# Performance work log

Measured on AMD Instinct MI355X. Metric: run time of the kernel, lower is better.

Reference implementation:

```python
import jax, jax.numpy as jnp
import numpy as np

NE = 64        # num experts
H = 1024       # hidden_size
F = 2048       # ffn_hidden_size per expert
T = 16384      # total tokens


def setup_inputs() -> dict:
    key = jax.random.key(0)
    k1, k2, k3 = jax.random.split(key, 3)
    x = jax.random.normal(k1, (T, H), jnp.float32)
    w1 = jax.random.normal(k2, (NE, F, H), jnp.float32) * 0.02
    w2 = jax.random.normal(k3, (NE, F, H), jnp.float32) * 0.02
    # ragged token counts per expert, summing exactly to T
    rng = np.random.default_rng(0)
    sizes = rng.multinomial(T, np.ones(NE) / NE)
    tokens_per_expert = jnp.asarray(sizes, jnp.int32)
    return {"x": x, "w1": w1, "w2": w2, "tokens_per_expert": tokens_per_expert}


def _grouped_gmm(x, w, sizes, trans_b=False):
    # grouped GEMM: per-expert segment of x multiplied by that expert's weight.
    # sizes are concrete host ints (group boundaries are static), so we emit
    # one GEMM per expert with static slices, matching gg.ops.gmm semantics.
    offs = np.concatenate([[0], np.cumsum(sizes)]).astype(np.int64)
    outs = []
    for e in range(len(sizes)):
        xe = x[int(offs[e]):int(offs[e + 1])]          # [n_e, k]
        we = w[e].T if trans_b else w[e]               # [k, n]
        outs.append(xe @ we)
    return jnp.concatenate(outs, axis=0)


def reference(x, w1, w2, tokens_per_expert):
    sizes = np.asarray(tokens_per_expert)
    h = _grouped_gmm(x, w1, sizes, trans_b=True)       # [T, F]
    h = jax.nn.gelu(h, approximate=False)              # torch F.gelu (exact erf)
    return _grouped_gmm(h, w2, sizes, trans_b=False)   # [T, H]
```

## Files before the change

### kernel.cpp

```cpp
#include <hip/hip_runtime.h>
#include <hip/hip_bf16.h>

#define NE 64
#define HDIM 1024
#define FDIM 2048
#define TDIM 16384

typedef __attribute__((ext_vector_type(8))) short short8;
typedef __attribute__((ext_vector_type(4))) float f32x4;
typedef unsigned short u16;
typedef unsigned int u32;

struct IC0 { static constexpr int v = 0; };
struct IC1 { static constexpr int v = 1; };

__device__ __forceinline__ u16 f2bf(float f) {
  return __bfloat16_as_ushort(__float2bfloat16(f));
}
__device__ __forceinline__ u32 pk2(float a, float b) {
  return (u32)f2bf(a) | ((u32)f2bf(b) << 16);
}
template<int N> __device__ __forceinline__ void waitv() {
  if constexpr (N == 2)       asm volatile("s_waitcnt vmcnt(2)" ::: "memory");
  else if constexpr (N == 4)  asm volatile("s_waitcnt vmcnt(4)" ::: "memory");
  else if constexpr (N == 8)  asm volatile("s_waitcnt vmcnt(8)" ::: "memory");
  else if constexpr (N == 10) asm volatile("s_waitcnt vmcnt(10)" ::: "memory");
}
__device__ __forceinline__ void waitl() {
  asm volatile("s_waitcnt lgkmcnt(0)" ::: "memory");
}

__global__ void k_prep(const int* __restrict__ tpe, int4* __restrict__ map,
                       int* __restrict__ nblocks) {
  if (threadIdx.x != 0 || blockIdx.x != 0) return;
  int off = 0, nb = 0;
  for (int e = 0; e < NE; ++e) {
    int n = tpe[e];
    for (int r = 0; r < n; r += 256) {
      int re = (r + 256 < n) ? (r + 256) : n;
      map[nb++] = make_int4(e, off + r, off + re, 0);
    }
    off += n;
  }
  *nblocks = nb;
}

__global__ void k_conv(const float4* __restrict__ in, uint2* __restrict__ out, int n4) {
  int stride = gridDim.x * blockDim.x;
  for (int i = blockIdx.x * blockDim.x + threadIdx.x; i < n4; i += stride) {
    float4 v = in[i];
    uint2 o;
    o.x = pk2(v.x, v.y);
    o.y = pk2(v.z, v.w);
    out[i] = o;
  }
}

template<int K, int N, bool GELU, int BMODE, int NY>
__global__ __launch_bounds__(512) void k_gemm(
    const u16* __restrict__ A, const float* __restrict__ Bf, void* __restrict__ C,
    const int4* __restrict__ map, const int* __restrict__ nblocks)
{
  const int mblk = (int)blockIdx.x / NY;
  const int nblk = (int)blockIdx.x % NY;
  if (mblk >= *nblocks) return;
  const int4 mi = map[mblk];
  const int e = mi.x, row0 = mi.y, rowend = mi.z;
  const int n0 = nblk << 7;
  const int NT = K / 32;
  constexpr int LB = (BMODE == 1) ? 2 : 8;

  __shared__ __align__(16) u16 sa[2][8192];
  __shared__ __align__(16) u16 sb[128 * 40];

  const int tid = threadIdx.x;
  const int wid = tid >> 6, lane = tid & 63;
  const int wr = wid >> 1, wc = wid & 1;
  const int fr = lane & 15, fq = lane >> 4;

  f32x4 acc[4][4];
#pragma unroll
  for (int m = 0; m < 4; ++m)
#pragma unroll
    for (int n = 0; n < 4; ++n) acc[m][n] = (f32x4)0.f;

  const float* B = Bf + (size_t)e * ((size_t)N * K);

  float4 rb1[2][2];
  float  rb2[2][8];
  const int bn  = tid & 127;
  const int oct = tid >> 7;

  auto issueA = [&](int t) {
    const int buf = t & 1;
#pragma unroll
    for (int i = 0; i < 2; ++i) {
      int slot = i * 512 + tid;
      int row = row0 + (slot >> 2);
      row = row < TDIM ? row : TDIM - 1;
      const u16* g = A + (size_t)row * K + t * 32 + (slot & 3) * 8;
      __builtin_amdgcn_global_load_lds(
          (const __attribute__((address_space(1))) u32*)g,
          (__attribute__((address_space(3))) u32*)(&sa[buf][i * 4096 + wid * 512]),
          16, 0, 0);
    }
  };
  auto loadB = [&](int t, auto ic) {
    constexpr int S = decltype(ic)::v;
    if constexpr (BMODE == 1) {
#pragma unroll
      for (int i = 0; i < 2; ++i) {
        int slot = i * 512 + tid;
        rb1[S][i] = *(const float4*)(B + (size_t)(n0 + (slot >> 3)) * K + t * 32 + (slot & 7) * 4);
      }
    } else {
      const float* src = B + (size_t)(t * 32 + oct * 8) * N + n0 + bn;
#pragma unroll
      for (int i = 0; i < 8; ++i) rb2[S][i] = src[(size_t)i * N];
    }
  };
  auto writeB = [&](auto ic) {
    constexpr int S = decltype(ic)::v;
    if constexpr (BMODE == 1) {
#pragma unroll
      for (int i = 0; i < 2; ++i) {
        int slot = i * 512 + tid;
        uint2 o;
        o.x = pk2(rb1[S][i].x, rb1[S][i].y);
        o.y = pk2(rb1[S][i].z, rb1[S][i].w);
        *(uint2*)(&sb[(slot >> 3) * 40 + (slot & 7) * 4]) = o;
      }
    } else {
      uint4 c;
      c.x = pk2(rb2[S][0], rb2[S][1]); c.y = pk2(rb2[S][2], rb2[S][3]);
      c.z = pk2(rb2[S][4], rb2[S][5]); c.w = pk2(rb2[S][6], rb2[S][7]);
      *(uint4*)(&sb[bn * 40 + oct * 8]) = c;
    }
  };

  auto body = [&](int t, auto icCur) {
    waitv<2 + LB>();
    waitl();
    __builtin_amdgcn_s_barrier();
    const int cur = t & 1;
    short8 av[4], bv[4];
#pragma unroll
    for (int m = 0; m < 4; ++m)
      av[m] = *(const short8*)(&sa[cur][(wr * 64 + m * 16 + fr) * 32 + fq * 8]);
#pragma unroll
    for (int n = 0; n < 4; ++n)
      bv[n] = *(const short8*)(&sb[(wc * 64 + n * 16 + fr) * 40 + fq * 8]);
    waitl();
    __builtin_amdgcn_sched_barrier(0);
    __builtin_amdgcn_s_barrier();
    if (t + 2 < NT) issueA(t + 2);
    if (t + 1 < NT) writeB(icCur);
    if (t + 3 < NT) loadB(t + 3, icCur);
    __builtin_amdgcn_sched_barrier(0);
#pragma unroll
    for (int m = 0; m < 4; ++m)
#pragma unroll
      for (int n = 0; n < 4; ++n)
        acc[m][n] = __builtin_amdgcn_mfma_f32_16x16x32_bf16(av[m], bv[n], acc[m][n], 0, 0, 0);
  };

  issueA(0);
  loadB(0, IC0{});
  loadB(1, IC1{});
  waitv<LB>();
  writeB(IC0{});
  issueA(1);
  loadB(2, IC0{});
  for (int t = 0; t < NT; t += 2) {
    body(t, IC1{});
    body(t + 1, IC0{});
  }

#pragma unroll
  for (int m = 0; m < 4; ++m) {
    const int rb = row0 + wr * 64 + m * 16 + fq * 4;
#pragma unroll
    for (int n = 0; n < 4; ++n) {
      const int col = n0 + wc * 64 + n * 16 + fr;
#pragma unroll
      for (int j = 0; j < 4; ++j) {
        int r = rb + j;
        if (r < rowend) {
          float vv = acc[m][n][j];
          if constexpr (GELU) {
            vv = 0.5f * vv * (1.f + erff(vv * 0.70710678118654752f));
            ((u16*)C)[(size_t)r * N + col] = f2bf(vv);
          } else {
            ((float*)C)[(size_t)r * N + col] = vv;
          }
        }
      }
    }
  }
}

extern "C" void kernel_launch(void* const* d_in, const int* in_sizes, int n_in,
                              void* d_out, int out_size, void* d_ws, size_t ws_size,
                              hipStream_t stream) {
  const float* x  = (const float*)d_in[0];
  const float* w1 = (const float*)d_in[1];
  const float* w2 = (const float*)d_in[2];
  const int*  tpe = (const int*)d_in[3];

  char* ws = (char*)d_ws;
  int4* map     = (int4*)ws;
  int*  nblocks = (int*)(ws + 4096);
  u16*  xb      = (u16*)(ws + 8192);
  u16*  hb      = xb + (size_t)TDIM * HDIM;

  k_prep<<<1, 64, 0, stream>>>(tpe, map, nblocks);
  k_conv<<<2048, 256, 0, stream>>>((const float4*)x, (uint2*)xb, (TDIM * HDIM) / 4);
  k_gemm<HDIM, FDIM, true,  1, 16><<<128 * 16, 512, 0, stream>>>(
      xb, w1, (void*)hb, map, nblocks);
  k_gemm<FDIM, HDIM, false, 2, 8><<<128 * 8, 512, 0, stream>>>(
      hb, w2, d_out, map, nblocks);
}
```

Measured before the change: 540.5 us.

## Double-buffer B tile, swizzle A LDS layout, drop mid-iteration barrier

Makes the B shared-memory tile double-buffered so the next B tile can be written while the current one is read. This removes the second barrier and lgkm wait inside each K iteration. The A tile now gets a prefetch distance of one instead of two, and its LDS layout is XOR-swizzled on both the global_load_lds writes and the fragment reads to reduce bank conflicts. Out-of-range prefetches are clamped to the last tile instead of skipped. This trades extra LDS use and redundant tail loads for fewer synchronization points. The reduced A lookahead and removed barrier raise the risk of read/write races on the shared buffers.

Measured after the change: 517.5 us. 4.3% less time.

```diff
diff --git a/kernel.cpp b/kernel.cpp
--- a/kernel.cpp
+++ b/kernel.cpp
@@ -22,9 +22,7 @@
 }
 template<int N> __device__ __forceinline__ void waitv() {
   if constexpr (N == 2)       asm volatile("s_waitcnt vmcnt(2)" ::: "memory");
-  else if constexpr (N == 4)  asm volatile("s_waitcnt vmcnt(4)" ::: "memory");
   else if constexpr (N == 8)  asm volatile("s_waitcnt vmcnt(8)" ::: "memory");
-  else if constexpr (N == 10) asm volatile("s_waitcnt vmcnt(10)" ::: "memory");
 }
 __device__ __forceinline__ void waitl() {
   asm volatile("s_waitcnt lgkmcnt(0)" ::: "memory");
@@ -71,7 +69,7 @@
   constexpr int LB = (BMODE == 1) ? 2 : 8;
 
   __shared__ __align__(16) u16 sa[2][8192];
-  __shared__ __align__(16) u16 sb[128 * 40];
+  __shared__ __align__(16) u16 sb[2][128 * 40];
 
   const int tid = threadIdx.x;
   const int wid = tid >> 6, lane = tid & 63;
@@ -91,14 +89,15 @@
   const int bn  = tid & 127;
   const int oct = tid >> 7;
 
-  auto issueA = [&](int t) {
-    const int buf = t & 1;
+  auto issueA = [&](int t, int buf) {
 #pragma unroll
     for (int i = 0; i < 2; ++i) {
       int slot = i * 512 + tid;
-      int row = row0 + (slot >> 2);
+      int r = slot >> 2, c = slot & 3;
+      int cs = c ^ ((r >> 1) & 3);
+      int row = row0 + r;
       row = row < TDIM ? row : TDIM - 1;
-      const u16* g = A + (size_t)row * K + t * 32 + (slot & 3) * 8;
+      const u16* g = A + (size_t)row * K + t * 32 + cs * 8;
       __builtin_amdgcn_global_load_lds(
           (const __attribute__((address_space(1))) u32*)g,
           (__attribute__((address_space(3))) u32*)(&sa[buf][i * 4096 + wid * 512]),
@@ -119,7 +118,7 @@
       for (int i = 0; i < 8; ++i) rb2[S][i] = src[(size_t)i * N];
     }
   };
-  auto writeB = [&](auto ic) {
+  auto writeB = [&](int buf, auto ic) {
     constexpr int S = decltype(ic)::v;
     if constexpr (BMODE == 1) {
 #pragma unroll
@@ -128,35 +127,33 @@
         uint2 o;
         o.x = pk2(rb1[S][i].x, rb1[S][i].y);
         o.y = pk2(rb1[S][i].z, rb1[S][i].w);
-        *(uint2*)(&sb[(slot >> 3) * 40 + (slot & 7) * 4]) = o;
+        *(uint2*)(&sb[buf][(slot >> 3) * 40 + (slot & 7) * 4]) = o;
       }
     } else {
       uint4 c;
       c.x = pk2(rb2[S][0], rb2[S][1]); c.y = pk2(rb2[S][2], rb2[S][3]);
       c.z = pk2(rb2[S][4], rb2[S][5]); c.w = pk2(rb2[S][6], rb2[S][7]);
-      *(uint4*)(&sb[bn * 40 + oct * 8]) = c;
+      *(uint4*)(&sb[buf][bn * 40 + oct * 8]) = c;
     }
   };
 
   auto body = [&](int t, auto icCur) {
-    waitv<2 + LB>();
+    waitv<LB>();
     waitl();
     __builtin_amdgcn_s_barrier();
-    const int cur = t & 1;
+    const int cur = t & 1, nxt = cur ^ 1;
     short8 av[4], bv[4];
 #pragma unroll
-    for (int m = 0; m < 4; ++m)
-      av[m] = *(const short8*)(&sa[cur][(wr * 64 + m * 16 + fr) * 32 + fq * 8]);
+    for (int m = 0; m < 4; ++m) {
+      const int row = wr * 64 + m * 16 + fr;
+      av[m] = *(const short8*)(&sa[cur][row * 32 + (fq ^ ((row >> 1) & 3)) * 8]);
+    }
 #pragma unroll
     for (int n = 0; n < 4; ++n)
-      bv[n] = *(const short8*)(&sb[(wc * 64 + n * 16 + fr) * 40 + fq * 8]);
-    waitl();
-    __builtin_amdgcn_sched_barrier(0);
-    __builtin_amdgcn_s_barrier();
-    if (t + 2 < NT) issueA(t + 2);
-    if (t + 1 < NT) writeB(icCur);
-    if (t + 3 < NT) loadB(t + 3, icCur);
-    __builtin_amdgcn_sched_barrier(0);
+      bv[n] = *(const short8*)(&sb[cur][(wc * 64 + n * 16 + fr) * 40 + fq * 8]);
+    issueA((t + 1 < NT) ? (t + 1) : (NT - 1), nxt);
+    writeB(nxt, icCur);
+    loadB((t + 3 < NT) ? (t + 3) : (NT - 1), icCur);
 #pragma unroll
     for (int m = 0; m < 4; ++m)
 #pragma unroll
@@ -164,12 +161,11 @@
         acc[m][n] = __builtin_amdgcn_mfma_f32_16x16x32_bf16(av[m], bv[n], acc[m][n], 0, 0, 0);
   };
 
-  issueA(0);
+  issueA(0, 0);
   loadB(0, IC0{});
   loadB(1, IC1{});
   waitv<LB>();
-  writeB(IC0{});
-  issueA(1);
+  writeB(0, IC0{});
   loadB(2, IC0{});
   for (int t = 0; t < NT; t += 2) {
     body(t, IC1{});
```
